# Performance work log

Measured on AMD Instinct MI355X. Metric: run time of the kernel, lower is better.

## Reference

```python
import jax, jax.numpy as jnp
import numpy as np

N_NODES = 50000
N_EDGES = 800000
IN_CH = 128
OUT_CH = 64
HEADS = 4
NEG_SLOPE = 0.2


def gat_layer(x, src, dst, W, a_src, a_dst, b, n):
    """One GATConv (PyG semantics, self-loops already in src/dst).
    x:[n,Fin], W:[Fin,H*C], a_src/a_dst:[H,C], b:[H*C]. Returns [n,H*C] (concat heads)."""
    H, C = a_src.shape
    h = (x @ W).reshape(n, H, C)                      # [n,H,C]
    alpha_s = jnp.einsum('nhc,hc->nh', h, a_src)      # [n,H]
    alpha_d = jnp.einsum('nhc,hc->nh', h, a_dst)
    e = jax.nn.leaky_relu(alpha_s[src] + alpha_d[dst], NEG_SLOPE)  # [E,H]
    m = jax.ops.segment_max(e, dst, num_segments=n)   # per-dst-node max (stable softmax)
    p = jnp.exp(e - m[dst])
    denom = jax.ops.segment_sum(p, dst, num_segments=n)
    alpha = p / (denom[dst] + 1e-16)                  # [E,H]
    out = jax.ops.segment_sum(h[src] * alpha[:, :, None], dst, num_segments=n)
    return out.reshape(n, H * C) + b


def setup_inputs() -> dict:
    key = jax.random.key(0)
    ks = jax.random.split(key, 10)
    x = jax.random.normal(ks[0], (N_NODES, IN_CH), dtype=jnp.float32)
    edge_index = jax.random.randint(ks[1], (2, N_EDGES), 0, N_NODES, dtype=jnp.int64)
    s = 0.05
    W1 = jax.random.normal(ks[2], (IN_CH, HEADS * OUT_CH), dtype=jnp.float32) * s
    a_src1 = jax.random.normal(ks[3], (HEADS, OUT_CH), dtype=jnp.float32) * s
    a_dst1 = jax.random.normal(ks[4], (HEADS, OUT_CH), dtype=jnp.float32) * s
    b1 = jnp.zeros((HEADS * OUT_CH,), dtype=jnp.float32)
    W2 = jax.random.normal(ks[5], (HEADS * OUT_CH, OUT_CH), dtype=jnp.float32) * s
    a_src2 = jax.random.normal(ks[6], (1, OUT_CH), dtype=jnp.float32) * s
    a_dst2 = jax.random.normal(ks[7], (1, OUT_CH), dtype=jnp.float32) * s
    b2 = jnp.zeros((OUT_CH,), dtype=jnp.float32)
    return {"x": x, "edge_index": edge_index, "W1": W1, "a_src1": a_src1,
            "a_dst1": a_dst1, "b1": b1, "W2": W2, "a_src2": a_src2,
            "a_dst2": a_dst2, "b2": b2}


def reference(x, edge_index, W1, a_src1, a_dst1, b1, W2, a_src2, a_dst2, b2):
    n = x.shape[0]
    # PyG GATConv adds self-loops by default
    loops = jnp.arange(n, dtype=edge_index.dtype)
    src = jnp.concatenate([edge_index[0], loops])
    dst = jnp.concatenate([edge_index[1], loops])
    h = jax.nn.relu(gat_layer(x, src, dst, W1, a_src1, a_dst1, b1, n))
    return gat_layer(h, src, dst, W2, a_src2, a_dst2, b2, n)
```

## Files before the change

kernel.cpp:

```cpp
#include <hip/hip_runtime.h>
#include <math.h>

#define N_NODES   50000
#define E0_EDGES  800000
#define E_TOT     (E0_EDGES + N_NODES)
#define FIN       128
#define F1        256
#define H1        4
#define C2        64
#define NEG_SLOPE 0.2f

#define NBX1      ((N_NODES + 63) / 64)
#define GEMM1_BLOCKS (NBX1 * 2)
#define SCAT_BLOCKS  ((E_TOT + 255) / 256)

typedef short bf16x8 __attribute__((ext_vector_type(8)));
typedef float f32x4  __attribute__((ext_vector_type(4)));

__device__ __forceinline__ unsigned short f2bf(float f) {
  unsigned u = __float_as_uint(f);
  u = (u + 0x7FFFu + ((u >> 16) & 1u)) >> 16;
  return (unsigned short)u;
}
__device__ __forceinline__ float bf2f(unsigned short h) {
  return __uint_as_float((unsigned)h << 16);
}
__device__ __forceinline__ float leaky(float v) {
  return v >= 0.f ? v : NEG_SLOPE * v;
}

__global__ __launch_bounds__(256) void deg_kernel(
    const int* __restrict__ ei, int* __restrict__ count,
    int* __restrict__ rank) {
  int e = blockIdx.x * 256 + threadIdx.x;
  if (e >= E_TOT) return;
  int dst = (e < E0_EDGES) ? ei[E0_EDGES + e] : (e - E0_EDGES);
  rank[e] = atomicAdd(&count[dst], 1);
}

__global__ __launch_bounds__(256) void scanA_kernel(
    const int* __restrict__ cnt, int* __restrict__ bsum, int n) {
  int i = blockIdx.x * 256 + threadIdx.x;
  int v = (i < n) ? cnt[i] : 0;
#pragma unroll
  for (int d = 1; d < 64; d <<= 1) v += __shfl_xor(v, d);
  __shared__ int ws[4];
  if ((threadIdx.x & 63) == 0) ws[threadIdx.x >> 6] = v;
  __syncthreads();
  if (threadIdx.x == 0) bsum[blockIdx.x] = ws[0] + ws[1] + ws[2] + ws[3];
}

__global__ __launch_bounds__(256) void scanB_kernel(
    const int* __restrict__ bsum, int* __restrict__ bexcl,
    int* __restrict__ off_n, int nb) {
  const int t = threadIdx.x, lane = t & 63, wid = t >> 6;
  int v = (t < nb) ? bsum[t] : 0;
  int sv = v;
#pragma unroll
  for (int d = 1; d < 64; d <<= 1) {
    int u = __shfl_up(sv, d);
    if (lane >= d) sv += u;
  }
  __shared__ int ws[4];
  if (lane == 63) ws[wid] = sv;
  __syncthreads();
  int add = 0;
  for (int k = 0; k < wid; ++k) add += ws[k];
  int incl = sv + add;
  if (t < nb) bexcl[t] = incl - v;
  if (t == 255) off_n[0] = incl;
}

__global__ __launch_bounds__(256) void scanC_kernel(
    const int* __restrict__ cnt, const int* __restrict__ bexcl,
    int* __restrict__ off, int n) {
  const int t = threadIdx.x, lane = t & 63, wid = t >> 6;
  int i = blockIdx.x * 256 + t;
  int v = (i < n) ? cnt[i] : 0;
  int sv = v;
#pragma unroll
  for (int d = 1; d < 64; d <<= 1) {
    int u = __shfl_up(sv, d);
    if (lane >= d) sv += u;
  }
  __shared__ int ws[4];
  if (lane == 63) ws[wid] = sv;
  __syncthreads();
  int add = 0;
  for (int k = 0; k < wid; ++k) add += ws[k];
  if (i < n) off[i] = sv + add - v + bexcl[blockIdx.x];
}

__global__ __launch_bounds__(256) void gemm1_scatter_kernel(
    const float* __restrict__ A, const float* __restrict__ B,
    unsigned short* __restrict__ C, float* __restrict__ as1,
    float* __restrict__ ad1, const float* __restrict__ a_s,
    const float* __restrict__ a_d, int M,
    const int* __restrict__ ei, const int* __restrict__ offset,
    const int* __restrict__ rank, int* __restrict__ csr_src) {
  constexpr int K = FIN, BN = 128, KP = K + 8, NF = BN / 16;
  __shared__ unsigned short BT[BN * KP];
  const int bid = blockIdx.x;

  if (bid >= GEMM1_BLOCKS) {
    int e = (bid - GEMM1_BLOCKS) * 256 + threadIdx.x;
    if (e >= E_TOT) return;
    int src, dst;
    if (e < E0_EDGES) { src = ei[e]; dst = ei[E0_EDGES + e]; }
    else              { src = e - E0_EDGES; dst = src; }
    csr_src[offset[dst] + rank[e]] = src;
    return;
  }

  const int bx = bid % NBX1;
  const int gy = bid / NBX1;
  const int tid = threadIdx.x, lane = tid & 63, wid = tid >> 6;
  const int n0 = gy * BN;

  for (int idx = tid; idx < K * (BN / 8); idx += 256) {
    int k = idx >> 4;
    int c = idx & 15;
    const float* src = &B[(size_t)k * F1 + n0 + c * 8];
    float4 lo = *reinterpret_cast<const float4*>(src);
    float4 hi = *reinterpret_cast<const float4*>(src + 4);
    int nb = c * 8;
    BT[(nb + 0) * KP + k] = f2bf(lo.x); BT[(nb + 1) * KP + k] = f2bf(lo.y);
    BT[(nb + 2) * KP + k] = f2bf(lo.z); BT[(nb + 3) * KP + k] = f2bf(lo.w);
    BT[(nb + 4) * KP + k] = f2bf(hi.x); BT[(nb + 5) * KP + k] = f2bf(hi.y);
    BT[(nb + 6) * KP + k] = f2bf(hi.z); BT[(nb + 7) * KP + k] = f2bf(hi.w);
  }
  __syncthreads();

  const int r0 = (bx * 4 + wid) * 16;
  if (r0 >= M) return;
  const int nlane = lane & 15;
  const int kg    = (lane >> 4) * 8;
  const int arow  = min(r0 + nlane, M - 1);

  f32x4 acc[NF];
#pragma unroll
  for (int nf = 0; nf < NF; ++nf) acc[nf] = (f32x4){0.f, 0.f, 0.f, 0.f};

  const float* ap = &A[(size_t)arow * K + kg];
#pragma unroll
  for (int kk = 0; kk < K; kk += 32) {
    float4 v0 = *reinterpret_cast<const float4*>(ap + kk);
    float4 v1 = *reinterpret_cast<const float4*>(ap + kk + 4);
    bf16x8 a;
    a[0] = (short)f2bf(v0.x); a[1] = (short)f2bf(v0.y);
    a[2] = (short)f2bf(v0.z); a[3] = (short)f2bf(v0.w);
    a[4] = (short)f2bf(v1.x); a[5] = (short)f2bf(v1.y);
    a[6] = (short)f2bf(v1.z); a[7] = (short)f2bf(v1.w);
#pragma unroll
    for (int nf = 0; nf < NF; ++nf) {
      bf16x8 b = *reinterpret_cast<const bf16x8*>(&BT[(nf * 16 + nlane) * KP + kk + kg]);
      acc[nf] = __builtin_amdgcn_mfma_f32_16x16x32_bf16(a, b, acc[nf], 0, 0, 0);
    }
  }

  const int crow = r0 + (lane >> 4) * 4;
#pragma unroll
  for (int nf = 0; nf < NF; ++nf) {
    const int cc = n0 + nf * 16 + nlane;
#pragma unroll
    for (int j = 0; j < 4; ++j) {
      int rr = crow + j;
      if (rr < M) C[(size_t)rr * F1 + cc] = f2bf(acc[nf][j]);
    }
  }

#pragma unroll
  for (int j = 0; j < 4; ++j) {
    float ps0 = 0.f, ps1 = 0.f, pd0 = 0.f, pd1 = 0.f;
#pragma unroll
    for (int nf = 0; nf < NF; ++nf) {
      int col = n0 + nf * 16 + nlane;
      float v = acc[nf][j];
      float sc = a_s[col], dc = a_d[col];
      if (nf < 4) { ps0 = fmaf(v, sc, ps0); pd0 = fmaf(v, dc, pd0); }
      else        { ps1 = fmaf(v, sc, ps1); pd1 = fmaf(v, dc, pd1); }
    }
#pragma unroll
    for (int d = 1; d < 16; d <<= 1) {
      ps0 += __shfl_xor(ps0, d); ps1 += __shfl_xor(ps1, d);
      pd0 += __shfl_xor(pd0, d); pd1 += __shfl_xor(pd1, d);
    }
    int row = crow + j;
    if (nlane == 0 && row < M) {
      float2 s2 = {ps0, ps1}, d2 = {pd0, pd1};
      *reinterpret_cast<float2*>(&as1[row * 4 + gy * 2]) = s2;
      *reinterpret_cast<float2*>(&ad1[row * 4 + gy * 2]) = d2;
    }
  }
}

__global__ __launch_bounds__(256) void w1_kernel(
    const float* __restrict__ as1, const float* __restrict__ ad1,
    const int* __restrict__ csr_src, const int* __restrict__ offset,
    float* __restrict__ w4, int n) {
  const int lane = threadIdx.x & 63;
  const int node = blockIdx.x * 4 + (threadIdx.x >> 6);
  if (node >= n) return;
  const int beg = offset[node], end = offset[node + 1];
  const float4 d4 = *reinterpret_cast<const float4*>(&ad1[node * H1]);
  for (int e = beg + lane; e < end; e += 64) {
    const int s = csr_src[e];
    const float4 s4 = *reinterpret_cast<const float4*>(&as1[s * H1]);
    float4 w;
    w.x = __expf(leaky(s4.x + d4.x));
    w.y = __expf(leaky(s4.y + d4.y));
    w.z = __expf(leaky(s4.z + d4.z));
    w.w = __expf(leaky(s4.w + d4.w));
    *reinterpret_cast<float4*>(&w4[(size_t)e * 4]) = w;
  }
}

__global__ __launch_bounds__(256) void gemm2_kernel(
    const unsigned short* __restrict__ A, const float* __restrict__ B,
    unsigned short* __restrict__ C, float* __restrict__ as2,
    float* __restrict__ ad2, const float* __restrict__ a_s,
    const float* __restrict__ a_d, int M) {
  constexpr int K = F1, BN = 64, KP = K + 8, NF = BN / 16;
  __shared__ unsigned short BT[BN * KP];
  const int tid = threadIdx.x, lane = tid & 63, wid = tid >> 6;

  for (int idx = tid; idx < K * (BN / 8); idx += 256) {
    int k = idx >> 3;
    int c = idx & 7;
    const float* src = &B[(size_t)k * C2 + c * 8];
    float4 lo = *reinterpret_cast<const float4*>(src);
    float4 hi = *reinterpret_cast<const float4*>(src + 4);
    int nb = c * 8;
    BT[(nb + 0) * KP + k] = f2bf(lo.x); BT[(nb + 1) * KP + k] = f2bf(lo.y);
    BT[(nb + 2) * KP + k] = f2bf(lo.z); BT[(nb + 3) * KP + k] = f2bf(lo.w);
    BT[(nb + 4) * KP + k] = f2bf(hi.x); BT[(nb + 5) * KP + k] = f2bf(hi.y);
    BT[(nb + 6) * KP + k] = f2bf(hi.z); BT[(nb + 7) * KP + k] = f2bf(hi.w);
  }
  __syncthreads();

  const int r0 = (blockIdx.x * 4 + wid) * 16;
  if (r0 >= M) return;
  const int nlane = lane & 15;
  const int kg    = (lane >> 4) * 8;
  const int arow  = min(r0 + nlane, M - 1);

  f32x4 acc[NF];
#pragma unroll
  for (int nf = 0; nf < NF; ++nf) acc[nf] = (f32x4){0.f, 0.f, 0.f, 0.f};

  const unsigned short* ap = &A[(size_t)arow * K + kg];
#pragma unroll
  for (int kk = 0; kk < K; kk += 32) {
    bf16x8 a = *reinterpret_cast<const bf16x8*>(ap + kk);
#pragma unroll
    for (int nf = 0; nf < NF; ++nf) {
      bf16x8 b = *reinterpret_cast<const bf16x8*>(&BT[(nf * 16 + nlane) * KP + kk + kg]);
      acc[nf] = __builtin_amdgcn_mfma_f32_16x16x32_bf16(a, b, acc[nf], 0, 0, 0);
    }
  }

  const int crow = r0 + (lane >> 4) * 4;
#pragma unroll
  for (int nf = 0; nf < NF; ++nf) {
    const int cc = nf * 16 + nlane;
#pragma unroll
    for (int j = 0; j < 4; ++j) {
      int rr = crow + j;
      if (rr < M) C[(size_t)rr * C2 + cc] = f2bf(acc[nf][j]);
    }
  }

#pragma unroll
  for (int j = 0; j < 4; ++j) {
    float ps = 0.f, pd = 0.f;
#pragma unroll
    for (int nf = 0; nf < NF; ++nf) {
      int col = nf * 16 + nlane;
      float v = acc[nf][j];
      ps = fmaf(v, a_s[col], ps);
      pd = fmaf(v, a_d[col], pd);
    }
#pragma unroll
    for (int d = 1; d < 16; d <<= 1) {
      ps += __shfl_xor(ps, d);
      pd += __shfl_xor(pd, d);
    }
    int row = crow + j;
    if (nlane == 0 && row < M) { as2[row] = ps; ad2[row] = pd; }
  }
}

__global__ __launch_bounds__(256) void aggregate1_kernel(
    const unsigned short* __restrict__ h1b, const float* __restrict__ w4,
    const int* __restrict__ csr_src, const int* __restrict__ offset,
    const float* __restrict__ b1, unsigned short* __restrict__ out1b, int n) {
  const int lane = threadIdx.x & 63;
  const int node = blockIdx.x * 4 + (threadIdx.x >> 6);
  if (node >= n) return;
  const int beg = offset[node], end = offset[node + 1];
  const int hl = lane >> 4;
  const unsigned loff = (unsigned)(lane * 4);

  float4 acc = make_float4(0.f, 0.f, 0.f, 0.f);
  float den = 0.f;
  int e = beg;
  for (; e + 7 < end; e += 8) {
    int s[8];
    float wv[8];
    ushort4 r[8];
#pragma unroll
    for (int i = 0; i < 8; ++i) s[i] = csr_src[e + i];
#pragma unroll
    for (int i = 0; i < 8; ++i) wv[i] = w4[(size_t)(e + i) * 4 + hl];
#pragma unroll
    for (int i = 0; i < 8; ++i)
      r[i] = *reinterpret_cast<const ushort4*>(h1b + (unsigned)(s[i] * F1) + loff);
#pragma unroll
    for (int i = 0; i < 8; ++i) {
      den += wv[i];
      acc.x = fmaf(wv[i], bf2f(r[i].x), acc.x);
      acc.y = fmaf(wv[i], bf2f(r[i].y), acc.y);
      acc.z = fmaf(wv[i], bf2f(r[i].z), acc.z);
      acc.w = fmaf(wv[i], bf2f(r[i].w), acc.w);
    }
  }
  for (; e < end; ++e) {
    const int s0 = csr_src[e];
    const float w = w4[(size_t)e * 4 + hl];
    den += w;
    const ushort4 r0 = *reinterpret_cast<const ushort4*>(h1b + (unsigned)(s0 * F1) + loff);
    acc.x = fmaf(w, bf2f(r0.x), acc.x);
    acc.y = fmaf(w, bf2f(r0.y), acc.y);
    acc.z = fmaf(w, bf2f(r0.z), acc.z);
    acc.w = fmaf(w, bf2f(r0.w), acc.w);
  }
  const float inv = 1.f / (den + 1e-16f);
  const float4 bb = *reinterpret_cast<const float4*>(&b1[lane * 4]);
  ushort4 ob;
  ob.x = f2bf(fmaxf(fmaf(acc.x, inv, bb.x), 0.f));
  ob.y = f2bf(fmaxf(fmaf(acc.y, inv, bb.y), 0.f));
  ob.z = f2bf(fmaxf(fmaf(acc.z, inv, bb.z), 0.f));
  ob.w = f2bf(fmaxf(fmaf(acc.w, inv, bb.w), 0.f));
  *reinterpret_cast<ushort4*>(&out1b[(size_t)node * F1 + lane * 4]) = ob;
}

__global__ __launch_bounds__(256) void aggregate2_kernel(
    const unsigned short* __restrict__ h2b, const float* __restrict__ as,
    const float* __restrict__ ad, const int* __restrict__ csr_src,
    const int* __restrict__ offset, const float* __restrict__ b2,
    float* __restrict__ out, int n) {
  const int lane = threadIdx.x & 63;
  const int node = blockIdx.x * 4 + (threadIdx.x >> 6);
  if (node >= n) return;
  const int beg = offset[node], end = offset[node + 1];
  const float adv = ad[node];

  float acc = 0.f;
  float den = 0.f;
  int e = beg;
  for (; e + 7 < end; e += 8) {
    int s[8];
    unsigned short r[8];
    float a[8];
#pragma unroll
    for (int i = 0; i < 8; ++i) s[i] = csr_src[e + i];
#pragma unroll
    for (int i = 0; i < 8; ++i) r[i] = h2b[(unsigned)(s[i] * C2) + lane];
#pragma unroll
    for (int i = 0; i < 8; ++i) a[i] = as[s[i]];
#pragma unroll
    for (int i = 0; i < 8; ++i) {
      const float w = __expf(leaky(a[i] + adv));
      den += w;
      acc = fmaf(w, bf2f(r[i]), acc);
    }
  }
  for (; e < end; ++e) {
    const int s0 = csr_src[e];
    const float w = __expf(leaky(as[s0] + adv));
    den += w;
    acc = fmaf(w, bf2f(h2b[(unsigned)(s0 * C2) + lane]), acc);
  }
  out[(size_t)node * C2 + lane] = fmaf(acc, 1.f / (den + 1e-16f), b2[lane]);
}

extern "C" void kernel_launch(void* const* d_in, const int* in_sizes, int n_in,
                              void* d_out, int out_size, void* d_ws, size_t ws_size,
                              hipStream_t stream) {
  const float* x      = (const float*)d_in[0];
  const int*   ei     = (const int*)d_in[1];
  const float* W1     = (const float*)d_in[2];
  const float* a_src1 = (const float*)d_in[3];
  const float* a_dst1 = (const float*)d_in[4];
  const float* b1     = (const float*)d_in[5];
  const float* W2     = (const float*)d_in[6];
  const float* a_src2 = (const float*)d_in[7];
  const float* a_dst2 = (const float*)d_in[8];
  const float* b2     = (const float*)d_in[9];
  float*       out    = (float*)d_out;

  const int n = N_NODES;
  const int nchunks = (n + 255) / 256;

  char* w = (char*)d_ws;
  unsigned short* h1b   = (unsigned short*)w; w += (size_t)n * F1 * 2;
  unsigned short* out1b = (unsigned short*)w; w += (size_t)n * F1 * 2;
  float*          w4    = (float*)w;          w += (size_t)E_TOT * 4 * 4;
  float*          as1   = (float*)w;          w += (size_t)n * H1 * 4;
  float*          ad1   = (float*)w;          w += (size_t)n * H1 * 4;
  float*          as2   = (float*)w;          w += 200192;
  float*          ad2   = (float*)w;          w += 200192;
  int*            cnt   = (int*)w;            w += 200192;
  int*            off   = (int*)w;            w += 200704;
  int*            bsum  = (int*)w;            w += 1024;
  int*            bexcl = (int*)w;            w += 1024;
  int*            rank  = (int*)w;            w += 3400192;
  int*            csr   = (int*)w;            w += 3400192;
  unsigned short* h2b   = h1b;

  hipMemsetAsync(cnt, 0, 200192, stream);
  deg_kernel<<<SCAT_BLOCKS, 256, 0, stream>>>(ei, cnt, rank);
  scanA_kernel<<<nchunks, 256, 0, stream>>>(cnt, bsum, n);
  scanB_kernel<<<1, 256, 0, stream>>>(bsum, bexcl, &off[n], nchunks);
  scanC_kernel<<<nchunks, 256, 0, stream>>>(cnt, bexcl, off, n);

  gemm1_scatter_kernel<<<GEMM1_BLOCKS + SCAT_BLOCKS, 256, 0, stream>>>(
      x, W1, h1b, as1, ad1, a_src1, a_dst1, n, ei, off, rank, csr);

  w1_kernel<<<(n + 3) / 4, 256, 0, stream>>>(as1, ad1, csr, off, w4, n);
  aggregate1_kernel<<<(n + 3) / 4, 256, 0, stream>>>(h1b, w4, csr, off, b1, out1b, n);

  gemm2_kernel<<<(n + 63) / 64, 256, 0, stream>>>(out1b, W2, h2b, as2, ad2,
                                                  a_src2, a_dst2, n);
  aggregate2_kernel<<<(n + 3) / 4, 256, 0, stream>>>(h2b, as2, ad2, csr, off, b2, out, n);
}
```

Before: 297.2 us.

## Replace three-pass scan with atomic-reserved offsets and fuse edge weights into aggregation

Replaces the three-kernel prefix scan with a single kernel. Each wavefront reserves its segment base through an atomicAdd on a global counter, so node offsets are no longer globally ordered, and segment ends are now taken from offset plus count. It also removes the separate w1 kernel and its per-edge weight buffer. aggregate1 now recomputes exp(leaky(as+ad)) per head while gathering, which cuts two launches and a large write/read of edge weights. The cost is redundant exp work across the 16 lanes that share a head, and a non-contiguous CSR layout whose locality depends on atomic order.

```diff
diff --git a/kernel.cpp b/kernel.cpp
--- a/kernel.cpp
+++ b/kernel.cpp
@@ -38,57 +38,22 @@
   rank[e] = atomicAdd(&count[dst], 1);
 }
 
-__global__ __launch_bounds__(256) void scanA_kernel(
-    const int* __restrict__ cnt, int* __restrict__ bsum, int n) {
-  int i = blockIdx.x * 256 + threadIdx.x;
+__global__ __launch_bounds__(256) void reserve_kernel(
+    const int* __restrict__ cnt, int* __restrict__ off,
+    int* __restrict__ total, int n) {
+  const int t = threadIdx.x, lane = t & 63;
+  int i = blockIdx.x * 256 + t;
   int v = (i < n) ? cnt[i] : 0;
-#pragma unroll
-  for (int d = 1; d < 64; d <<= 1) v += __shfl_xor(v, d);
-  __shared__ int ws[4];
-  if ((threadIdx.x & 63) == 0) ws[threadIdx.x >> 6] = v;
-  __syncthreads();
-  if (threadIdx.x == 0) bsum[blockIdx.x] = ws[0] + ws[1] + ws[2] + ws[3];
-}
-
-__global__ __launch_bounds__(256) void scanB_kernel(
-    const int* __restrict__ bsum, int* __restrict__ bexcl,
-    int* __restrict__ off_n, int nb) {
-  const int t = threadIdx.x, lane = t & 63, wid = t >> 6;
-  int v = (t < nb) ? bsum[t] : 0;
   int sv = v;
 #pragma unroll
   for (int d = 1; d < 64; d <<= 1) {
     int u = __shfl_up(sv, d);
     if (lane >= d) sv += u;
   }
-  __shared__ int ws[4];
-  if (lane == 63) ws[wid] = sv;
-  __syncthreads();
-  int add = 0;
-  for (int k = 0; k < wid; ++k) add += ws[k];
-  int incl = sv + add;
-  if (t < nb) bexcl[t] = incl - v;
-  if (t == 255) off_n[0] = incl;
-}
-
-__global__ __launch_bounds__(256) void scanC_kernel(
-    const int* __restrict__ cnt, const int* __restrict__ bexcl,
-    int* __restrict__ off, int n) {
-  const int t = threadIdx.x, lane = t & 63, wid = t >> 6;
-  int i = blockIdx.x * 256 + t;
-  int v = (i < n) ? cnt[i] : 0;
-  int sv = v;
-#pragma unroll
-  for (int d = 1; d < 64; d <<= 1) {
-    int u = __shfl_up(sv, d);
-    if (lane >= d) sv += u;
-  }
-  __shared__ int ws[4];
-  if (lane == 63) ws[wid] = sv;
-  __syncthreads();
-  int add = 0;
-  for (int k = 0; k < wid; ++k) add += ws[k];
-  if (i < n) off[i] = sv + add - v + bexcl[blockIdx.x];
+  int base = 0;
+  if (lane == 63) base = atomicAdd(total, sv);
+  base = __shfl(base, 63);
+  if (i < n) off[i] = base + sv - v;
 }
 
 __global__ __launch_bounds__(256) void gemm1_scatter_kernel(
@@ -194,27 +159,6 @@
   }
 }
 
-__global__ __launch_bounds__(256) void w1_kernel(
-    const float* __restrict__ as1, const float* __restrict__ ad1,
-    const int* __restrict__ csr_src, const int* __restrict__ offset,
-    float* __restrict__ w4, int n) {
-  const int lane = threadIdx.x & 63;
-  const int node = blockIdx.x * 4 + (threadIdx.x >> 6);
-  if (node >= n) return;
-  const int beg = offset[node], end = offset[node + 1];
-  const float4 d4 = *reinterpret_cast<const float4*>(&ad1[node * H1]);
-  for (int e = beg + lane; e < end; e += 64) {
-    const int s = csr_src[e];
-    const float4 s4 = *reinterpret_cast<const float4*>(&as1[s * H1]);
-    float4 w;
-    w.x = __expf(leaky(s4.x + d4.x));
-    w.y = __expf(leaky(s4.y + d4.y));
-    w.z = __expf(leaky(s4.z + d4.z));
-    w.w = __expf(leaky(s4.w + d4.w));
-    *reinterpret_cast<float4*>(&w4[(size_t)e * 4]) = w;
-  }
-}
-
 __global__ __launch_bounds__(256) void gemm2_kernel(
     const unsigned short* __restrict__ A, const float* __restrict__ B,
     unsigned short* __restrict__ C, float* __restrict__ as2,
@@ -291,14 +235,16 @@
 }
 
 __global__ __launch_bounds__(256) void aggregate1_kernel(
-    const unsigned short* __restrict__ h1b, const float* __restrict__ w4,
-    const int* __restrict__ csr_src, const int* __restrict__ offset,
+    const unsigned short* __restrict__ h1b, const float* __restrict__ as,
+    const float* __restrict__ ad, const int* __restrict__ csr_src,
+    const int* __restrict__ offset, const int* __restrict__ cnt,
     const float* __restrict__ b1, unsigned short* __restrict__ out1b, int n) {
   const int lane = threadIdx.x & 63;
   const int node = blockIdx.x * 4 + (threadIdx.x >> 6);
   if (node >= n) return;
-  const int beg = offset[node], end = offset[node + 1];
+  const int beg = offset[node], end = beg + cnt[node];
   const int hl = lane >> 4;
+  const float adh = ad[node * H1 + hl];
   const unsigned loff = (unsigned)(lane * 4);
 
   float4 acc = make_float4(0.f, 0.f, 0.f, 0.f);
@@ -306,27 +252,28 @@
   int e = beg;
   for (; e + 7 < end; e += 8) {
     int s[8];
-    float wv[8];
     ushort4 r[8];
+    float a[8];
 #pragma unroll
     for (int i = 0; i < 8; ++i) s[i] = csr_src[e + i];
-#pragma unroll
-    for (int i = 0; i < 8; ++i) wv[i] = w4[(size_t)(e + i) * 4 + hl];
 #pragma unroll
     for (int i = 0; i < 8; ++i)
       r[i] = *reinterpret_cast<const ushort4*>(h1b + (unsigned)(s[i] * F1) + loff);
 #pragma unroll
+    for (int i = 0; i < 8; ++i) a[i] = as[s[i] * H1 + hl];
+#pragma unroll
     for (int i = 0; i < 8; ++i) {
-      den += wv[i];
-      acc.x = fmaf(wv[i], bf2f(r[i].x), acc.x);
-      acc.y = fmaf(wv[i], bf2f(r[i].y), acc.y);
-      acc.z = fmaf(wv[i], bf2f(r[i].z), acc.z);
-      acc.w = fmaf(wv[i], bf2f(r[i].w), acc.w);
+      const float w = __expf(leaky(a[i] + adh));
+      den += w;
+      acc.x = fmaf(w, bf2f(r[i].x), acc.x);
+      acc.y = fmaf(w, bf2f(r[i].y), acc.y);
+      acc.z = fmaf(w, bf2f(r[i].z), acc.z);
+      acc.w = fmaf(w, bf2f(r[i].w), acc.w);
     }
   }
   for (; e < end; ++e) {
     const int s0 = csr_src[e];
-    const float w = w4[(size_t)e * 4 + hl];
+    const float w = __expf(leaky(as[s0 * H1 + hl] + adh));
     den += w;
     const ushort4 r0 = *reinterpret_cast<const ushort4*>(h1b + (unsigned)(s0 * F1) + loff);
     acc.x = fmaf(w, bf2f(r0.x), acc.x);
@@ -347,12 +294,12 @@
 __global__ __launch_bounds__(256) void aggregate2_kernel(
     const unsigned short* __restrict__ h2b, const float* __restrict__ as,
     const float* __restrict__ ad, const int* __restrict__ csr_src,
-    const int* __restrict__ offset, const float* __restrict__ b2,
-    float* __restrict__ out, int n) {
+    const int* __restrict__ offset, const int* __restrict__ cnt,
+    const float* __restrict__ b2, float* __restrict__ out, int n) {
   const int lane = threadIdx.x & 63;
   const int node = blockIdx.x * 4 + (threadIdx.x >> 6);
   if (node >= n) return;
-  const int beg = offset[node], end = offset[node + 1];
+  const int beg = offset[node], end = beg + cnt[node];
   const float adv = ad[node];
 
   float acc = 0.f;
@@ -405,32 +352,29 @@
   char* w = (char*)d_ws;
   unsigned short* h1b   = (unsigned short*)w; w += (size_t)n * F1 * 2;
   unsigned short* out1b = (unsigned short*)w; w += (size_t)n * F1 * 2;
-  float*          w4    = (float*)w;          w += (size_t)E_TOT * 4 * 4;
   float*          as1   = (float*)w;          w += (size_t)n * H1 * 4;
   float*          ad1   = (float*)w;          w += (size_t)n * H1 * 4;
   float*          as2   = (float*)w;          w += 200192;
   float*          ad2   = (float*)w;          w += 200192;
   int*            cnt   = (int*)w;            w += 200192;
-  int*            off   = (int*)w;            w += 200704;
-  int*            bsum  = (int*)w;            w += 1024;
-  int*            bexcl = (int*)w;            w += 1024;
+  int*            total = (int*)w;            w += 1024;
+  int*            off   = (int*)w;            w += 200192;
   int*            rank  = (int*)w;            w += 3400192;
   int*            csr   = (int*)w;            w += 3400192;
   unsigned short* h2b   = h1b;
 
-  hipMemsetAsync(cnt, 0, 200192, stream);
+  hipMemsetAsync(cnt, 0, 200192 + 1024, stream);
   deg_kernel<<<SCAT_BLOCKS, 256, 0, stream>>>(ei, cnt, rank);
-  scanA_kernel<<<nchunks, 256, 0, stream>>>(cnt, bsum, n);
-  scanB_kernel<<<1, 256, 0, stream>>>(bsum, bexcl, &off[n], nchunks);
-  scanC_kernel<<<nchunks, 256, 0, stream>>>(cnt, bexcl, off, n);
+  reserve_kernel<<<nchunks, 256, 0, stream>>>(cnt, off, total, n);
 
   gemm1_scatter_kernel<<<GEMM1_BLOCKS + SCAT_BLOCKS, 256, 0, stream>>>(
       x, W1, h1b, as1, ad1, a_src1, a_dst1, n, ei, off, rank, csr);
 
-  w1_kernel<<<(n + 3) / 4, 256, 0, stream>>>(as1, ad1, csr, off, w4, n);
-  aggregate1_kernel<<<(n + 3) / 4, 256, 0, stream>>>(h1b, w4, csr, off, b1, out1b, n);
+  aggregate1_kernel<<<(n + 3) / 4, 256, 0, stream>>>(
+      h1b, as1, ad1, csr, off, cnt, b1, out1b, n);
 
   gemm2_kernel<<<(n + 63) / 64, 256, 0, stream>>>(out1b, W2, h2b, as2, ad2,
                                                   a_src2, a_dst2, n);
-  aggregate2_kernel<<<(n + 3) / 4, 256, 0, stream>>>(h2b, as2, ad2, csr, off, b2, out, n);
-}
+  aggregate2_kernel<<<(n + 3) / 4, 256, 0, stream>>>(
+      h2b, as2, ad2, csr, off, cnt, b2, out, n);
+}
```

New measurement: 292.8 us. About the same (-1.5%).
